# Kernel tuning notes

Measured on AMD Instinct MI355X. Metric: run time of the kernel, lower is better.

## Reference

```python
import jax, jax.numpy as jnp
import numpy as np

EPS = 1e-9
N = 32768


def signed_area(poly):
    # poly: [..., K, 2] -> signed shoelace area (CCW positive)
    x = poly[..., 0]; y = poly[..., 1]
    x2 = jnp.roll(x, -1, axis=-1); y2 = jnp.roll(y, -1, axis=-1)
    return 0.5 * jnp.sum(x * y2 - x2 * y, axis=-1)


def convex_hull_pad(pts):
    # pts: [K,2] -> [K,2] CCW convex-hull vertices, padded by repeating the last hull vertex.
    K = pts.shape[0]
    a = pts[:, None, None, :]; b = pts[None, :, None, :]; c = pts[None, None, :, :]
    # cr[i,j,k] = cross(p_j - p_i, p_k - p_i); edge i->j on hull iff all points left of it
    cr = (b - a)[..., 0] * (c - a)[..., 1] - (b - a)[..., 1] * (c - a)[..., 0]
    not_eye = ~jnp.eye(K, dtype=bool)
    is_edge = jnp.all(cr >= -1e-7, axis=2) & not_eye
    on_hull = jnp.any(is_edge, axis=1)
    w = on_hull.astype(pts.dtype)
    cen = (pts * w[:, None]).sum(0) / jnp.maximum(w.sum(), 1.0)
    ang = jnp.arctan2(pts[:, 1] - cen[1], pts[:, 0] - cen[0])
    order = jnp.argsort(jnp.where(on_hull, ang, jnp.inf))  # hull verts first, CCW by angle
    sp = pts[order]; sv = on_hull[order]
    last = sp[jnp.maximum(on_hull.sum() - 1, 0)]
    return jnp.where(sv[:, None], sp, last[None, :])


def clip_convex(subject, clip):
    # Sutherland-Hodgman: subject [S,2] CCW polygon (trailing duplicate padding OK),
    # clip [C,2] CCW convex polygon. Fixed-size, jit-friendly.
    S = subject.shape[0]
    poly = subject
    b_all = jnp.roll(clip, -1, axis=0)
    for i in range(clip.shape[0]):  # static small loop over clip edges
        a = clip[i]; b = b_all[i]
        p = poly; q = jnp.roll(poly, -1, axis=0)
        ex = b[0] - a[0]; ey = b[1] - a[1]
        dp = ex * (p[:, 1] - a[1]) - ey * (p[:, 0] - a[0])
        dq = ex * (q[:, 1] - a[1]) - ey * (q[:, 0] - a[0])
        in_p = dp >= 0; in_q = dq >= 0
        denom = dp - dq
        t = dp / jnp.where(jnp.abs(denom) < EPS, EPS, denom)
        inter = p + t[:, None] * (q - p)
        cand = jnp.stack([inter, q], axis=1).reshape(2 * S, 2)
        flags = jnp.stack([in_p != in_q, in_q], axis=1).reshape(2 * S)
        order = jnp.argsort(1 - flags.astype(jnp.int32))  # stable: valid verts first, order kept
        cand = cand[order]; flags = flags[order]
        last = cand[jnp.maximum(flags.sum() - 1, 0)]
        poly = jnp.where(flags[:, None], cand, last[None, :])[:S]
    return poly


def giou_one(pred18, target8):
    P = pred18.reshape(9, 2)
    T = target8.reshape(4, 2)
    sa = signed_area(T)
    T_ccw = jnp.where(sa < 0, T[::-1], T)
    hullA = convex_hull_pad(P)  # [9,2]
    areaA = jnp.abs(signed_area(hullA))
    areaB = jnp.abs(sa)
    # pad subject to 16 verts (clipped 9-gon has <= 13 verts)
    subj = jnp.concatenate([hullA, jnp.broadcast_to(hullA[-1], (7, 2))], axis=0)
    inter = jnp.abs(signed_area(clip_convex(subj, T_ccw)))
    union = areaA + areaB - inter
    hullC = convex_hull_pad(jnp.concatenate([P, T], axis=0))  # enclosing hull of 13 pts
    areaC = jnp.abs(signed_area(hullC))
    return inter / jnp.maximum(union, EPS) - (areaC - union) / jnp.maximum(areaC, EPS)


def setup_inputs():
    key = jax.random.key(0)
    k1, k2, k3, k4, k5, k6 = jax.random.split(key, 6)
    # pred: 9 rep-points scattered around a random center
    ctr = jax.random.uniform(k1, (N, 1, 2), minval=0.0, maxval=1024.0)
    off = jax.random.normal(k2, (N, 9, 2)) * 24.0
    pred = (ctr + off).reshape(N, 18).astype(jnp.float32)
    # target: rotated-rectangle corners [N,8]
    tc = jax.random.uniform(k3, (N, 1, 2), minval=0.0, maxval=1024.0)
    wh = jax.random.uniform(k4, (N, 1, 2), minval=16.0, maxval=128.0)
    ang = jax.random.uniform(k5, (N, 1), minval=0.0, maxval=2.0 * np.pi)
    unit = jnp.array([[-0.5, -0.5], [0.5, -0.5], [0.5, 0.5], [-0.5, 0.5]], jnp.float32)
    xy = unit[None] * wh  # [N,4,2]
    ca = jnp.cos(ang); sn = jnp.sin(ang)
    rx = xy[..., 0] * ca - xy[..., 1] * sn
    ry = xy[..., 0] * sn + xy[..., 1] * ca
    target = (jnp.stack([rx, ry], axis=-1) + tc).reshape(N, 8).astype(jnp.float32)
    weight = jax.random.uniform(k6, (N,), dtype=jnp.float32)
    return {"pred": pred, "target": target, "weight": weight}


def reference(pred, target, weight):
    gious = jax.vmap(giou_one)(pred, target)  # [N]
    loss = (1.0 - gious) * weight
    return jnp.mean(loss)  # reduction='mean', loss_weight=1.0
```

## Files before the change

kernel.cpp:

```cpp
#include <hip/hip_runtime.h>
#include <math.h>

#define EPSD 1e-9

template<int K>
__device__ __forceinline__ void sortxy(double (&x)[K], double (&y)[K]) {
#pragma unroll
    for (int r = 0; r < K; r++) {
#pragma unroll
        for (int j = (r & 1); j + 1 < K; j += 2) {
            bool sw = (x[j] > x[j + 1]) || ((x[j] == x[j + 1]) && (y[j] > y[j + 1]));
            double tx = x[j], ty = y[j];
            x[j] = sw ? x[j + 1] : tx;
            y[j] = sw ? y[j + 1] : ty;
            x[j + 1] = sw ? tx : x[j + 1];
            y[j + 1] = sw ? ty : y[j + 1];
        }
    }
}

template<int K>
__device__ __forceinline__ int chain_hull(const double (&sx)[K], const double (&sy)[K],
                                          double2* Hb) {
    int k = 0;
    double t1x = 0.0, t1y = 0.0, t2x = 0.0, t2y = 0.0;
#define PUSH_(PX, PY)                                                         \
    {                                                                         \
        if (k >= 2) Hb[(k - 2) * 64] = make_double2(t2x, t2y);                \
        t2x = t1x; t2y = t1y; t1x = (PX); t1y = (PY); k++;                    \
    }
#define POPS_(PX, PY, LIM)                                                    \
    while (k >= (LIM) &&                                                      \
           ((t1x - t2x) * ((PY) - t2y) - (t1y - t2y) * ((PX) - t2x)) <= 0.0) {\
        k--;                                                                  \
        t1x = t2x; t1y = t2y;                                                 \
        if (k >= 2) { double2 v_ = Hb[(k - 2) * 64]; t2x = v_.x; t2y = v_.y; }\
    }
#pragma unroll
    for (int i = 0; i < K; i++) {
        double px = sx[i], py = sy[i];
        POPS_(px, py, 2);
        PUSH_(px, py);
    }
    const int lim = k + 1;
#pragma unroll
    for (int i = K - 2; i >= 0; i--) {
        double px = sx[i], py = sy[i];
        POPS_(px, py, lim);
        PUSH_(px, py);
    }
#undef PUSH_
#undef POPS_
    if (k >= 2) Hb[(k - 2) * 64] = make_double2(t2x, t2y);
    Hb[(k - 1) * 64] = make_double2(t1x, t1y);
    return k - 1;
}

__global__ __launch_bounds__(64)
void giou_kernel(const float* __restrict__ pred,
                 const float* __restrict__ target,
                 const float* __restrict__ weight,
                 double* __restrict__ ws,
                 int n) {
    __shared__ double2 Hs[16 * 64];
    double2* Hb = &Hs[threadIdx.x];
    const int lane = threadIdx.x;
    const int odd = lane & 1;
    const int i0 = blockIdx.x * 32 + (lane >> 1);
    const bool valid = i0 < n;
    const int i = valid ? i0 : (n > 0 ? n - 1 : 0);

    double Tx[4], Ty[4];
    {
        const float4* tp = (const float4*)target + (size_t)i * 2;
        float4 t0 = tp[0], t1 = tp[1];
        Tx[0] = t0.x; Ty[0] = t0.y; Tx[1] = t0.z; Ty[1] = t0.w;
        Tx[2] = t1.x; Ty[2] = t1.y; Tx[3] = t1.z; Ty[3] = t1.w;
    }
    double saT = 0.5 * ((Tx[0] * Ty[1] - Tx[1] * Ty[0]) + (Tx[1] * Ty[2] - Tx[2] * Ty[1]) +
                        (Tx[2] * Ty[3] - Tx[3] * Ty[2]) + (Tx[3] * Ty[0] - Tx[0] * Ty[3]));
    double areaB = fabs(saT);
    bool rev = saT < 0.0;
    double tcx[4], tcy[4];
#pragma unroll
    for (int k = 0; k < 4; k++) {
        tcx[k] = rev ? Tx[3 - k] : Tx[k];
        tcy[k] = rev ? Ty[3 - k] : Ty[k];
    }

    double X[13], Y[13];
    {
        const float2* pp = (const float2*)pred + (size_t)i * 9;
#pragma unroll
        for (int k = 0; k < 9; k++) { float2 v = pp[k]; X[k] = v.x; Y[k] = v.y; }
    }
#pragma unroll
    for (int k = 0; k < 4; k++) {
        X[9 + k] = odd ? Tx[k] : X[0];
        Y[9 + k] = odd ? Ty[k] : Y[0];
    }

    sortxy<13>(X, Y);
    int m = chain_hull<13>(X, Y, Hb);

    double qx[16], qy[16];
#pragma unroll
    for (int j = 0; j < 16; j++) {
        int idx = (j < m - 1) ? j : (m - 1);
        double2 v = Hb[idx * 64];
        qx[j] = v.x; qy[j] = v.y;
    }
    double sA = 0.0;
#pragma unroll
    for (int s = 0; s < 16; s++) {
        const int s1 = (s + 1) & 15;
        sA += qx[s] * qy[s1] - qx[s1] * qy[s];
    }
    double area = fabs(0.5 * sA);
    double other = __shfl_xor(area, 1, 64);
    double areaA = odd ? other : area;
    double areaC = odd ? area : other;

#pragma unroll
    for (int e = 0; e < 4; e++) {
        double ax = tcx[e], ay = tcy[e];
        double bx = tcx[(e + 1) & 3], by = tcy[(e + 1) & 3];
        double ex_ = bx - ax, ey_ = by - ay;

        double d[16];
#pragma unroll
        for (int s = 0; s < 16; s++) d[s] = ex_ * (qy[s] - ay) - ey_ * (qx[s] - ax);

        int nk = 0;
        double lastx = 0.0, lasty = 0.0, fcx = 0.0, fcy = 0.0;
#pragma unroll
        for (int s = 0; s < 16; s++) {
            const int s1 = (s + 1) & 15;
            double dp = d[s], dq = d[s1];
            bool inp = dp >= 0.0, inq = dq >= 0.0;
            double den = dp - dq;
            double dd = (fabs(den) < EPSD) ? EPSD : den;
            double t = dp / dd;
            double ix = qx[s] + t * (qx[s1] - qx[s]);
            double iy = qy[s] + t * (qy[s1] - qy[s]);
            if (s == 0) { fcx = ix; fcy = iy; }
            bool f1 = inp != inq;
            if (f1) {
                if (nk < 16) Hb[nk * 64] = make_double2(ix, iy);
                nk++;
                lastx = ix; lasty = iy;
            }
            if (inq) {
                if (nk < 16) Hb[nk * 64] = make_double2(qx[s1], qy[s1]);
                nk++;
                lastx = qx[s1]; lasty = qy[s1];
            }
        }
        bool any = nk > 0;
        double lx = any ? lastx : fcx;
        double ly = any ? lasty : fcy;
#pragma unroll
        for (int j = 0; j < 16; j++) {
            double2 v = Hb[j * 64];
            bool keep = j < nk;
            qx[j] = keep ? v.x : lx;
            qy[j] = keep ? v.y : ly;
        }
    }
    double sI = 0.0;
#pragma unroll
    for (int s = 0; s < 16; s++) {
        const int s1 = (s + 1) & 15;
        sI += qx[s] * qy[s1] - qx[s1] * qy[s];
    }
    double interA = fabs(0.5 * sI);

    double uni = areaA + areaB - interA;
    double giou = interA / fmax(uni, EPSD) - (areaC - uni) / fmax(areaC, EPSD);
    double loss = (1.0 - giou) * (double)weight[i];
    double contrib = (!odd && valid) ? loss : 0.0;

#pragma unroll
    for (int off = 32; off > 0; off >>= 1) contrib += __shfl_down(contrib, off, 64);
    if (lane == 0) ws[blockIdx.x] = contrib;
}

__global__ __launch_bounds__(256)
void reduce_kernel(const double* __restrict__ ws, float* __restrict__ out,
                   int nb, double invN) {
    int t = threadIdx.x;
    double s = 0.0;
    for (int j = t; j < nb; j += 256) s += ws[j];
#pragma unroll
    for (int off = 32; off > 0; off >>= 1) s += __shfl_down(s, off, 64);
    __shared__ double red[4];
    if ((t & 63) == 0) red[t >> 6] = s;
    __syncthreads();
    if (t == 0) out[0] = (float)((red[0] + red[1] + red[2] + red[3]) * invN);
}

extern "C" void kernel_launch(void* const* d_in, const int* in_sizes, int n_in,
                              void* d_out, int out_size, void* d_ws, size_t ws_size,
                              hipStream_t stream) {
    const float* pred = (const float*)d_in[0];
    const float* target = (const float*)d_in[1];
    const float* weight = (const float*)d_in[2];
    float* out = (float*)d_out;
    double* ws = (double*)d_ws;
    int n = in_sizes[2];

    int grid = (n + 31) / 32;
    giou_kernel<<<grid, 64, 0, stream>>>(pred, target, weight, ws, n);
    reduce_kernel<<<1, 256, 0, stream>>>(ws, out, grid, 1.0 / (double)n);
}
```

Measured before the change: 82.37 us.

## Replace Sutherland-Hodgman clipping with split edge-clipping Green's theorem intersection area

Drops the 4-pass Sutherland-Hodgman clip over a 16-slot padded polygon. Intersection area is now a boundary integral: the even lane clips each hull edge against the target quad (Cyrus-Beck style lo/hi) and the odd lane clips each target edge against the pred hull. The two partial sums are combined with a shuffle. The hull area loop now runs only over the m real vertices instead of 16 padded slots. This removes many divides, LDS stores and selects, but adds a __syncthreads, data-dependent loops and lane divergence. Degenerate or collinear edge cases may differ slightly from the reference.

```diff
diff --git a/kernel.cpp b/kernel.cpp
--- a/kernel.cpp
+++ b/kernel.cpp
@@ -103,80 +103,93 @@
     sortxy<13>(X, Y);
     int m = chain_hull<13>(X, Y, Hb);
 
-    double qx[16], qy[16];
-#pragma unroll
-    for (int j = 0; j < 16; j++) {
-        int idx = (j < m - 1) ? j : (m - 1);
-        double2 v = Hb[idx * 64];
-        qx[j] = v.x; qy[j] = v.y;
-    }
-    double sA = 0.0;
-#pragma unroll
-    for (int s = 0; s < 16; s++) {
-        const int s1 = (s + 1) & 15;
-        sA += qx[s] * qy[s1] - qx[s1] * qy[s];
-    }
-    double area = fabs(0.5 * sA);
+    double area;
+    {
+        double2 h0 = Hb[0];
+        double px = h0.x, py = h0.y, s = 0.0;
+#pragma unroll 1
+        for (int j = 1; j < m; j++) {
+            double2 c = Hb[j * 64];
+            s += px * c.y - c.x * py;
+            px = c.x; py = c.y;
+        }
+        s += px * h0.y - h0.x * py;
+        area = fabs(0.5 * s);
+    }
     double other = __shfl_xor(area, 1, 64);
     double areaA = odd ? other : area;
     double areaC = odd ? area : other;
-
-#pragma unroll
-    for (int e = 0; e < 4; e++) {
-        double ax = tcx[e], ay = tcy[e];
-        double bx = tcx[(e + 1) & 3], by = tcy[(e + 1) & 3];
-        double ex_ = bx - ax, ey_ = by - ay;
-
-        double d[16];
-#pragma unroll
-        for (int s = 0; s < 16; s++) d[s] = ex_ * (qy[s] - ay) - ey_ * (qx[s] - ax);
-
-        int nk = 0;
-        double lastx = 0.0, lasty = 0.0, fcx = 0.0, fcy = 0.0;
-#pragma unroll
-        for (int s = 0; s < 16; s++) {
-            const int s1 = (s + 1) & 15;
-            double dp = d[s], dq = d[s1];
-            bool inp = dp >= 0.0, inq = dq >= 0.0;
-            double den = dp - dq;
-            double dd = (fabs(den) < EPSD) ? EPSD : den;
-            double t = dp / dd;
-            double ix = qx[s] + t * (qx[s1] - qx[s]);
-            double iy = qy[s] + t * (qy[s1] - qy[s]);
-            if (s == 0) { fcx = ix; fcy = iy; }
-            bool f1 = inp != inq;
-            if (f1) {
-                if (nk < 16) Hb[nk * 64] = make_double2(ix, iy);
-                nk++;
-                lastx = ix; lasty = iy;
-            }
-            if (inq) {
-                if (nk < 16) Hb[nk * 64] = make_double2(qx[s1], qy[s1]);
-                nk++;
-                lastx = qx[s1]; lasty = qy[s1];
-            }
-        }
-        bool any = nk > 0;
-        double lx = any ? lastx : fcx;
-        double ly = any ? lasty : fcy;
-#pragma unroll
-        for (int j = 0; j < 16; j++) {
-            double2 v = Hb[j * 64];
-            bool keep = j < nk;
-            qx[j] = keep ? v.x : lx;
-            qy[j] = keep ? v.y : ly;
-        }
-    }
-    double sI = 0.0;
-#pragma unroll
-    for (int s = 0; s < 16; s++) {
-        const int s1 = (s + 1) & 15;
-        sI += qx[s] * qy[s1] - qx[s1] * qy[s];
-    }
-    double interA = fabs(0.5 * sI);
-
-    double uni = areaA + areaB - interA;
-    double giou = interA / fmax(uni, EPSD) - (areaC - uni) / fmax(areaC, EPSD);
+    int mo = __shfl_xor(m, 1, 64);
+    const int mA = odd ? mo : m;
+    __syncthreads();
+    const double2* HA = odd ? &Hs[lane - 1] : Hb;
+
+    double S = 0.0;
+    if (!odd) {
+#pragma unroll 1
+        for (int j = 0; j < mA; j++) {
+            double2 p = HA[j * 64];
+            int j1 = (j + 1 == mA) ? 0 : j + 1;
+            double2 q = HA[j1 * 64];
+            double lo = 0.0, hi = 1.0;
+#pragma unroll
+            for (int e = 0; e < 4; e++) {
+                double ax = tcx[e], ay = tcy[e];
+                int e1 = (e + 1) & 3;
+                double ex_ = tcx[e1] - ax, ey_ = tcy[e1] - ay;
+                double s0 = ex_ * (p.y - ay) - ey_ * (p.x - ax);
+                double s1 = ex_ * (q.y - ay) - ey_ * (q.x - ax);
+                bool in0 = s0 >= 0.0, in1 = s1 >= 0.0;
+                if (!in0 && !in1) { lo = 1.0; hi = 0.0; }
+                else if (in0 != in1) {
+                    double t = s0 / (s0 - s1);
+                    if (!in0) lo = fmax(lo, t); else hi = fmin(hi, t);
+                }
+            }
+            if (lo < hi) {
+                double dx_ = q.x - p.x, dy_ = q.y - p.y;
+                double A0x = p.x + lo * dx_, A0y = p.y + lo * dy_;
+                double B0x = p.x + hi * dx_, B0y = p.y + hi * dy_;
+                S += A0x * B0y - B0x * A0y;
+            }
+        }
+    } else if (mA >= 2) {
+        double lo[4] = {0.0, 0.0, 0.0, 0.0}, hi[4] = {1.0, 1.0, 1.0, 1.0};
+#pragma unroll 1
+        for (int j = 0; j < mA; j++) {
+            double2 a = HA[j * 64];
+            int j1 = (j + 1 == mA) ? 0 : j + 1;
+            double2 b = HA[j1 * 64];
+            double ex_ = b.x - a.x, ey_ = b.y - a.y;
+#pragma unroll
+            for (int k = 0; k < 4; k++) {
+                int k1 = (k + 1) & 3;
+                double s0 = ex_ * (tcy[k] - a.y) - ey_ * (tcx[k] - a.x);
+                double s1 = ex_ * (tcy[k1] - a.y) - ey_ * (tcx[k1] - a.x);
+                bool in0 = s0 >= 0.0, in1 = s1 >= 0.0;
+                if (!in0 && !in1) { lo[k] = 1.0; hi[k] = 0.0; }
+                else if (in0 != in1) {
+                    double t = s0 / (s0 - s1);
+                    if (!in0) lo[k] = fmax(lo[k], t); else hi[k] = fmin(hi[k], t);
+                }
+            }
+        }
+#pragma unroll
+        for (int k = 0; k < 4; k++) {
+            if (lo[k] < hi[k]) {
+                int k1 = (k + 1) & 3;
+                double dx_ = tcx[k1] - tcx[k], dy_ = tcy[k1] - tcy[k];
+                double A0x = tcx[k] + lo[k] * dx_, A0y = tcy[k] + lo[k] * dy_;
+                double B0x = tcx[k] + hi[k] * dx_, B0y = tcy[k] + hi[k] * dy_;
+                S += A0x * B0y - B0x * A0y;
+            }
+        }
+    }
+    double So = __shfl_xor(S, 1, 64);
+    double inter = fabs(0.5 * (S + So));
+
+    double uni = areaA + areaB - inter;
+    double giou = inter / fmax(uni, EPSD) - (areaC - uni) / fmax(areaC, EPSD);
     double loss = (1.0 - giou) * (double)weight[i];
     double contrib = (!odd && valid) ? loss : 0.0;
 
```

Result: no change. 81.02 us (-1.6%).
